# Kernel tuning notes

Measured on AMD Instinct MI355X. Metric: run time of the kernel, lower is better.

Reference implementation:

```python
import jax, jax.numpy as jnp
import numpy as np

HIDDEN_DIM = 2048
NUM_HEADS = 16
HEAD_DIM = HIDDEN_DIM // NUM_HEADS


def setup_inputs() -> dict:
    key = jax.random.key(0)
    ks = jax.random.split(key, 5)
    B, S, D = 1, 4096, HIDDEN_DIM
    scale = 1.0 / np.sqrt(D)
    x = jax.random.normal(ks[0], (B, S, D), dtype=jnp.float32)
    w_q = jax.random.normal(ks[1], (D, D), dtype=jnp.float32) * scale
    w_k = jax.random.normal(ks[2], (D, D), dtype=jnp.float32) * scale
    w_v = jax.random.normal(ks[3], (D, D), dtype=jnp.float32) * scale
    w_o = jax.random.normal(ks[4], (D, D), dtype=jnp.float32) * scale
    return {"x": x, "w_q": w_q, "w_k": w_k, "w_v": w_v, "w_o": w_o, "causal": 1}


def reference(x, w_q, w_k, w_v, w_o, causal):
    B, S, D = x.shape
    H, Dh = NUM_HEADS, HEAD_DIM
    sm_scale = 1.0 / np.sqrt(Dh)

    # projections (x @ W.T)
    q = jnp.einsum('bsd,ed->bse', x, w_q).reshape(B, S, H, Dh).transpose(0, 2, 1, 3)
    k = jnp.einsum('bsd,ed->bse', x, w_k).reshape(B, S, H, Dh).transpose(0, 2, 1, 3)
    v = jnp.einsum('bsd,ed->bse', x, w_v).reshape(B, S, H, Dh).transpose(0, 2, 1, 3)

    # attention scores [B, H, S, S]; flash online-softmax == standard softmax
    scores = jnp.einsum('bhqd,bhkd->bhqk', q, k) * sm_scale
    if causal:
        qpos = jnp.arange(S)[:, None]
        kpos = jnp.arange(S)[None, :]
        scores = jnp.where(qpos >= kpos, scores, -jnp.inf)
    probs = jax.nn.softmax(scores, axis=-1)
    o = jnp.einsum('bhqk,bhkd->bhqd', probs, v)  # [B, H, S, Dh]
    o = o.transpose(0, 2, 1, 3).reshape(B, S, D)
    return jnp.einsum('bsd,ed->bse', o, w_o)
```

## Files before the change

### kernel.cpp

```cpp
#include <hip/hip_runtime.h>
#include <stdint.h>

typedef __bf16 bf16_t;
typedef __bf16 bf16x8 __attribute__((ext_vector_type(8)));
typedef __bf16 bf16x4 __attribute__((ext_vector_type(4)));
typedef float  f32x4  __attribute__((ext_vector_type(4)));

static constexpr int S  = 4096;
static constexpr int D  = 2048;
static constexpr int H  = 16;
static constexpr int DH = 128;

__device__ __forceinline__ bf16x8 ld8(const bf16_t* p) { return *(const bf16x8*)p; }
__device__ __forceinline__ bf16x8 ld8c(const float* p) {
  const f32x4 a = *(const f32x4*)p;
  const f32x4 b = *(const f32x4*)(p + 4);
  bf16x8 r;
  r[0] = (bf16_t)a[0]; r[1] = (bf16_t)a[1]; r[2] = (bf16_t)a[2]; r[3] = (bf16_t)a[3];
  r[4] = (bf16_t)b[0]; r[5] = (bf16_t)b[1]; r[6] = (bf16_t)b[2]; r[7] = (bf16_t)b[3];
  return r;
}

__device__ __forceinline__ void async_ld16(const bf16_t* g, bf16_t* lds) {
  __builtin_amdgcn_global_load_lds(
      (const __attribute__((address_space(1))) uint32_t*)g,
      (__attribute__((address_space(3))) uint32_t*)lds, 16, 0, 0);
}

__global__ __launch_bounds__(256) void cvt_kernel(
    const float* __restrict__ x,  const float* __restrict__ wq,
    const float* __restrict__ wk, const float* __restrict__ wv,
    const float* __restrict__ wo,
    bf16_t* __restrict__ xb,  bf16_t* __restrict__ wqb,
    bf16_t* __restrict__ wkb, bf16_t* __restrict__ wvb,
    bf16_t* __restrict__ wob) {
  const int z = blockIdx.z;
  const float* src; bf16_t* dst; size_t off = 0;
  if      (z == 0) { src = x;  dst = xb;  off = 0; }
  else if (z == 1) { src = x;  dst = xb;  off = 4194304; }
  else if (z == 2) { src = wq; dst = wqb; }
  else if (z == 3) { src = wk; dst = wkb; }
  else if (z == 4) { src = wv; dst = wvb; }
  else             { src = wo; dst = wob; }
  const size_t i = off + ((size_t)blockIdx.x * 256 + threadIdx.x) * 8;
  *(bf16x8*)(dst + i) = ld8c(src + i);
}

template <typename TC, bool TR>
__device__ __forceinline__ void gemm_async(const bf16_t* __restrict__ A,
                                           const bf16_t* __restrict__ W,
                                           TC* __restrict__ C) {
  constexpr int K  = D;
  constexpr int BK = 32;
  __shared__ __align__(16) bf16_t Ash[128 * BK];
  __shared__ __align__(16) bf16_t Bsh[128 * BK];
  const int tid = threadIdx.x;
  const int w = tid >> 6, lane = tid & 63;
  const int c = lane & 15, g = lane >> 4;
  const int wm = w >> 1, wn = w & 1;
  const int rowBase = blockIdx.y * 128;
  const int colBase = blockIdx.x * 128;

  f32x4 acc[4][4] = {};

  for (int k0 = 0; k0 < K; k0 += BK) {
    __syncthreads();
    #pragma unroll
    for (int r = 0; r < 2; ++r) {
      const int cid = r * 256 + tid;
      const int row = cid >> 2, q = cid & 3;
      async_ld16(A + (size_t)(rowBase + row) * K + k0 + q * 8,
                 Ash + r * 2048 + w * 512);
      async_ld16(W + (size_t)(colBase + row) * K + k0 + q * 8,
                 Bsh + r * 2048 + w * 512);
    }
    __syncthreads();

    bf16x8 af[4], bf[4];
    #pragma unroll
    for (int i = 0; i < 4; ++i) af[i] = ld8(Ash + (wm * 64 + i * 16 + c) * BK + g * 8);
    #pragma unroll
    for (int j = 0; j < 4; ++j) bf[j] = ld8(Bsh + (wn * 64 + j * 16 + c) * BK + g * 8);
    #pragma unroll
    for (int i = 0; i < 4; ++i)
      #pragma unroll
      for (int j = 0; j < 4; ++j)
        acc[i][j] = __builtin_amdgcn_mfma_f32_16x16x32_bf16(af[i], bf[j], acc[i][j], 0, 0, 0);
  }

  #pragma unroll
  for (int i = 0; i < 4; ++i)
    #pragma unroll
    for (int j = 0; j < 4; ++j) {
      if (TR) {
        const int col  = colBase + wn * 64 + j * 16 + c;
        const int row0 = rowBase + wm * 64 + i * 16 + g * 4;
        bf16x4 v;
        #pragma unroll
        for (int r = 0; r < 4; ++r) v[r] = (bf16_t)acc[i][j][r];
        *(bf16x4*)((bf16_t*)C + (size_t)col * S + row0) = v;
      } else {
        #pragma unroll
        for (int r = 0; r < 4; ++r) {
          const int row = rowBase + wm * 64 + i * 16 + g * 4 + r;
          const int col = colBase + wn * 64 + j * 16 + c;
          C[(size_t)row * D + col] = (TC)acc[i][j][r];
        }
      }
    }
}

__global__ __launch_bounds__(256) void qkv_gemm_bf16(
    const bf16_t* __restrict__ X,
    const bf16_t* __restrict__ Wq, const bf16_t* __restrict__ Wk,
    const bf16_t* __restrict__ Wv,
    bf16_t* __restrict__ Qo, bf16_t* __restrict__ Ko, bf16_t* __restrict__ VTo) {
  if (blockIdx.z == 0)      gemm_async<bf16_t, false>(X, Wq, Qo);
  else if (blockIdx.z == 1) gemm_async<bf16_t, false>(X, Wk, Ko);
  else                      gemm_async<bf16_t, true >(X, Wv, VTo);
}

__global__ __launch_bounds__(256) void out_gemm_bf16(
    const bf16_t* __restrict__ A, const bf16_t* __restrict__ W,
    float* __restrict__ C) {
  gemm_async<float, false>(A, W, C);
}

__global__ __launch_bounds__(512, 2) void attn_kernel(
    const bf16_t* __restrict__ Q, const bf16_t* __restrict__ Kb,
    const bf16_t* __restrict__ VTg, bf16_t* __restrict__ O,
    const int* __restrict__ causal_p, int* __restrict__ ctr) {
  __shared__ __align__(16) bf16_t smem[40960];
  bf16_t* const KB0 = smem;
  bf16_t* const VB0 = smem + 16384;
  bf16_t* const Psh = smem + 32768;
  int* const item_sp = (int*)(smem + 40958);

  const int tid = threadIdx.x, w = tid >> 6, lane = tid & 63;
  const int c = lane & 15, g = lane >> 4;
  const int wq = w >> 1, wk = w & 1;
  const int causal = causal_p[0];
  constexpr float QS = 0.08838834764831845f * 1.4426950408889634f;

  int knA[2], qK8[2], dVA[2], qV8[2];
  #pragma unroll
  for (int r = 0; r < 2; ++r) {
    const int cid = r * 512 + tid;
    knA[r] = cid >> 4; qK8[r] = (((cid & 15) ^ (knA[r] & 7)) << 3);
    dVA[r] = cid >> 3; qV8[r] = (((cid & 7) ^ (dVA[r] & 7)) << 3);
  }

  bf16_t* const Pw = Psh + w * 1024;
  const int psw = (c >> 1) & 3;

  while (true) {
    if (tid == 0) *item_sp = atomicAdd(ctr, 1);
    __syncthreads();
    const int it = *item_sp;
    if (it >= 512) break;
    const int t = causal ? (31 - (it >> 4)) : (it >> 4);
    const int h = it & 15;
    const int qrow0 = t * 128 + wq * 32;
    const int ktiles = causal ? (2 * t + 2) : (S / 64);

    const bf16_t* kSrc[2];
    const bf16_t* vSrc[2];
    #pragma unroll
    for (int r = 0; r < 2; ++r) {
      kSrc[r] = Kb + (size_t)knA[r] * D + h * DH + qK8[r];
      vSrc[r] = VTg + (size_t)(h * DH + dVA[r]) * S + qV8[r];
    }
    #pragma unroll
    for (int r = 0; r < 2; ++r) {
      async_ld16(kSrc[r], KB0 + r * 4096 + w * 512);
      async_ld16(vSrc[r], VB0 + r * 4096 + w * 512);
      kSrc[r] += (size_t)64 * D;
      vSrc[r] += 64;
    }

    bf16x8 qf[2][4];
    #pragma unroll
    for (int i = 0; i < 2; ++i)
      #pragma unroll
      for (int kf = 0; kf < 4; ++kf) {
        const bf16x8 raw = ld8(Q + (size_t)(qrow0 + i * 16 + c) * D + h * DH + kf * 32 + g * 8);
        bf16x8 sc;
        #pragma unroll
        for (int e = 0; e < 8; ++e) sc[e] = (bf16_t)((float)raw[e] * QS);
        qf[i][kf] = sc;
      }

    f32x4 o_acc[2][8] = {};
    float psum[2] = {0.0f, 0.0f};

    __syncthreads();

    int cur = 0;
    for (int kt = 0; kt < ktiles; ++kt) {
      if (kt + 1 < ktiles) {
        const int alt = cur ^ 1;
        #pragma unroll
        for (int r = 0; r < 2; ++r) {
          async_ld16(kSrc[r], KB0 + alt * 8192 + r * 4096 + w * 512);
          async_ld16(vSrc[r], VB0 + alt * 8192 + r * 4096 + w * 512);
          kSrc[r] += (size_t)64 * D;
          vSrc[r] += 64;
        }
      }

      const bf16_t* const KB = KB0 + cur * 8192;
      const bf16_t* const VB = VB0 + cur * 8192;
      const int kb = kt * 64 + wk * 32;

      const bool active = !causal || (kb <= qrow0 + 31);
      if (active) {
        __builtin_amdgcn_s_setprio(1);
        #pragma unroll
        for (int nf = 0; nf < 2; ++nf) {
          const int rr = wk * 32 + nf * 16 + c;
          bf16x8 kk[4];
          #pragma unroll
          for (int kf = 0; kf < 4; ++kf)
            kk[kf] = ld8(KB + rr * 128 + ((((kf << 2) + g) ^ (rr & 7)) << 3));
          #pragma unroll
          for (int i = 0; i < 2; ++i) {
            f32x4 s = {};
            #pragma unroll
            for (int kf = 0; kf < 4; ++kf)
              s = __builtin_amdgcn_mfma_f32_16x16x32_bf16(kk[kf], qf[i][kf], s, 0, 0, 0);
            if (causal && (kb + nf * 16 + 15 > qrow0 + i * 16)) {
              #pragma unroll
              for (int r_ = 0; r_ < 4; ++r_)
                if (kb + nf * 16 + g * 4 + r_ > qrow0 + i * 16 + c) s[r_] = -1e30f;
            }
            bf16x4 pq;
            #pragma unroll
            for (int r_ = 0; r_ < 4; ++r_) {
              const float pv = exp2f(s[r_]);
              psum[i] += pv;
              pq[r_] = (bf16_t)pv;
            }
            const int p  = (nf << 1) | (g >> 1);
            const int pp = ((p ^ psw) << 1) | (g & 1);
            *(bf16x4*)(Pw + i * 512 + c * 32 + pp * 4) = pq;
          }
        }

        bf16x8 pf[2];
        #pragma unroll
        for (int i = 0; i < 2; ++i)
          pf[i] = ld8(Pw + i * 512 + c * 32 + ((g ^ psw) << 3));
        #pragma unroll
        for (int nf = 0; nf < 8; ++nf) {
          const int dl = nf * 16 + c;
          const bf16x8 vf = ld8(VB + dl * 64 + ((((wk << 2) + g) ^ (dl & 7)) << 3));
          o_acc[0][nf] = __builtin_amdgcn_mfma_f32_16x16x32_bf16(pf[0], vf, o_acc[0][nf], 0, 0, 0);
          o_acc[1][nf] = __builtin_amdgcn_mfma_f32_16x16x32_bf16(pf[1], vf, o_acc[1][nf], 0, 0, 0);
        }
        __builtin_amdgcn_s_setprio(0);
      }

      __syncthreads();
      cur ^= 1;
    }

    float* const slot = (float*)smem + (size_t)(wq * 64 + lane) * 72;
    if (wk == 1) {
      #pragma unroll
      for (int i = 0; i < 2; ++i)
        #pragma unroll
        for (int nf = 0; nf < 8; ++nf)
          *(f32x4*)(slot + (i * 8 + nf) * 4) = o_acc[i][nf];
      slot[64] = psum[0];
      slot[65] = psum[1];
    }
    __syncthreads();
    if (wk == 0) {
      #pragma unroll
      for (int i = 0; i < 2; ++i)
        #pragma unroll
        for (int nf = 0; nf < 8; ++nf)
          o_acc[i][nf] += *(const f32x4*)(slot + (i * 8 + nf) * 4);
      psum[0] += slot[64];
      psum[1] += slot[65];
      #pragma unroll
      for (int i = 0; i < 2; ++i) {
        float v = psum[i];
        v += __shfl_xor(v, 16); v += __shfl_xor(v, 32);
        #pragma unroll
        for (int r_ = 0; r_ < 4; ++r_) {
          const float inv = 1.0f / __shfl(v, g * 4 + r_, 64);
          const int row = qrow0 + i * 16 + g * 4 + r_;
          #pragma unroll
          for (int nf = 0; nf < 8; ++nf)
            O[(size_t)row * D + h * DH + nf * 16 + c] = (bf16_t)(o_acc[i][nf][r_] * inv);
        }
      }
    }
  }
}

extern "C" void kernel_launch(void* const* d_in, const int* in_sizes, int n_in,
                              void* d_out, int out_size, void* d_ws, size_t ws_size,
                              hipStream_t stream) {
  const float* x  = (const float*)d_in[0];
  const float* wq = (const float*)d_in[1];
  const float* wk = (const float*)d_in[2];
  const float* wv = (const float*)d_in[3];
  const float* wo = (const float*)d_in[4];
  const int* causal = (const int*)d_in[5];
  float* out = (float*)d_out;

  bf16_t* Qb  = (bf16_t*)d_ws;
  bf16_t* Kb  = Qb + (size_t)S * D;
  bf16_t* VTb = Kb + (size_t)S * D;
  bf16_t* Ob  = VTb + (size_t)S * D;
  bf16_t* xb  = Ob + (size_t)S * D;
  bf16_t* wqb = xb + (size_t)S * D;
  bf16_t* wkb = wqb + (size_t)D * D;
  bf16_t* wvb = wkb + (size_t)D * D;
  bf16_t* wob = wvb + (size_t)D * D;
  int*    ctr = (int*)(wob + (size_t)D * D);

  hipMemsetAsync(ctr, 0, sizeof(int), stream);

  dim3 blk(256);
  cvt_kernel<<<dim3(2048, 1, 6), blk, 0, stream>>>(x, wq, wk, wv, wo,
                                                   xb, wqb, wkb, wvb, wob);
  qkv_gemm_bf16<<<dim3(D / 128, S / 128, 3), blk, 0, stream>>>(xb, wqb, wkb, wvb,
                                                               Qb, Kb, VTb);
  attn_kernel<<<dim3(384), dim3(512), 0, stream>>>(Qb, Kb, VTb, Ob, causal, ctr);
  out_gemm_bf16<<<dim3(D / 128, S / 128), blk, 0, stream>>>(Ob, wob, out);
}
```

Measured before the change: 431.5 us.

## Fuse Q/K/V projections into one GEMM kernel sharing the X tile

Replaces the three-way blockIdx.z split of the QKV projection with a single kernel in which each block loads its X tile once and multiplies it against the Wq, Wk and Wv tiles, keeping three accumulator sets. This cuts redundant global and LDS traffic for X and launches a third as many blocks. In exchange each thread holds 192 accumulator registers, which may hurt occupancy or cause spills. The loop is single-buffered with a short BK, so latency hiding may be weaker than in the previous gemm_async path.

```diff
diff --git a/kernel.cpp b/kernel.cpp
--- a/kernel.cpp
+++ b/kernel.cpp
@@ -110,14 +110,73 @@
     }
 }
 
-__global__ __launch_bounds__(256) void qkv_gemm_bf16(
+__global__ __launch_bounds__(256, 2) void qkv_gemm_fused(
     const bf16_t* __restrict__ X,
     const bf16_t* __restrict__ Wq, const bf16_t* __restrict__ Wk,
     const bf16_t* __restrict__ Wv,
     bf16_t* __restrict__ Qo, bf16_t* __restrict__ Ko, bf16_t* __restrict__ VTo) {
-  if (blockIdx.z == 0)      gemm_async<bf16_t, false>(X, Wq, Qo);
-  else if (blockIdx.z == 1) gemm_async<bf16_t, false>(X, Wk, Ko);
-  else                      gemm_async<bf16_t, true >(X, Wv, VTo);
+  constexpr int K  = D;
+  constexpr int BK = 32;
+  __shared__ __align__(16) bf16_t Ash[128 * BK];
+  __shared__ __align__(16) bf16_t Bsh[3][128 * BK];
+  const int tid = threadIdx.x;
+  const int w = tid >> 6, lane = tid & 63;
+  const int c = lane & 15, g = lane >> 4;
+  const int wm = w >> 1, wn = w & 1;
+  const int rowBase = blockIdx.y * 128;
+  const int colBase = blockIdx.x * 128;
+
+  f32x4 acc[3][4][4] = {};
+
+  for (int k0 = 0; k0 < K; k0 += BK) {
+    __syncthreads();
+    #pragma unroll
+    for (int r = 0; r < 2; ++r) {
+      const int cid = r * 256 + tid;
+      const int row = cid >> 2, q = cid & 3;
+      const size_t aoff = (size_t)(rowBase + row) * K + k0 + q * 8;
+      const size_t boff = (size_t)(colBase + row) * K + k0 + q * 8;
+      async_ld16(X  + aoff, Ash    + r * 2048 + w * 512);
+      async_ld16(Wq + boff, Bsh[0] + r * 2048 + w * 512);
+      async_ld16(Wk + boff, Bsh[1] + r * 2048 + w * 512);
+      async_ld16(Wv + boff, Bsh[2] + r * 2048 + w * 512);
+    }
+    __syncthreads();
+
+    bf16x8 af[4];
+    #pragma unroll
+    for (int i = 0; i < 4; ++i) af[i] = ld8(Ash + (wm * 64 + i * 16 + c) * BK + g * 8);
+    #pragma unroll
+    for (int m = 0; m < 3; ++m) {
+      bf16x8 bf[4];
+      #pragma unroll
+      for (int j = 0; j < 4; ++j) bf[j] = ld8(Bsh[m] + (wn * 64 + j * 16 + c) * BK + g * 8);
+      #pragma unroll
+      for (int i = 0; i < 4; ++i)
+        #pragma unroll
+        for (int j = 0; j < 4; ++j)
+          acc[m][i][j] = __builtin_amdgcn_mfma_f32_16x16x32_bf16(af[i], bf[j], acc[m][i][j], 0, 0, 0);
+    }
+  }
+
+  #pragma unroll
+  for (int i = 0; i < 4; ++i)
+    #pragma unroll
+    for (int j = 0; j < 4; ++j) {
+      #pragma unroll
+      for (int r = 0; r < 4; ++r) {
+        const int row = rowBase + wm * 64 + i * 16 + g * 4 + r;
+        const int col = colBase + wn * 64 + j * 16 + c;
+        Qo[(size_t)row * D + col] = (bf16_t)acc[0][i][j][r];
+        Ko[(size_t)row * D + col] = (bf16_t)acc[1][i][j][r];
+      }
+      const int colv  = colBase + wn * 64 + j * 16 + c;
+      const int row0v = rowBase + wm * 64 + i * 16 + g * 4;
+      bf16x4 v;
+      #pragma unroll
+      for (int r = 0; r < 4; ++r) v[r] = (bf16_t)acc[2][i][j][r];
+      *(bf16x4*)(VTo + (size_t)colv * S + row0v) = v;
+    }
 }
 
 __global__ __launch_bounds__(256) void out_gemm_bf16(
@@ -327,8 +386,8 @@
   dim3 blk(256);
   cvt_kernel<<<dim3(2048, 1, 6), blk, 0, stream>>>(x, wq, wk, wv, wo,
                                                    xb, wqb, wkb, wvb, wob);
-  qkv_gemm_bf16<<<dim3(D / 128, S / 128, 3), blk, 0, stream>>>(xb, wqb, wkb, wvb,
-                                                               Qb, Kb, VTb);
+  qkv_gemm_fused<<<dim3(D / 128, S / 128), blk, 0, stream>>>(xb, wqb, wkb, wvb,
+                                                             Qb, Kb, VTb);
   attn_kernel<<<dim3(384), dim3(512), 0, stream>>>(Qb, Kb, VTb, Ob, causal, ctr);
   out_gemm_bf16<<<dim3(D / 128, S / 128), blk, 0, stream>>>(Ob, wob, out);
 }
```

Result: faster. 407.2 us (median of 2 runs) (-5.6%).
